# Kernel tuning notes

Hardware: AMD Instinct MI355X
Metric: run time of the kernel (lower is better)

Reference implementation:

```python
import jax, jax.numpy as jnp
import numpy as np

D, M, B, K = 512, 512, 8, 16
EPS = 1e-8
LAMBDA = 1.0
BALANCE_COEFF = 0.0


def _l2_normalize(x, axis=-1):
    n = jnp.linalg.norm(x, axis=axis, keepdims=True)
    return x / jnp.maximum(n, EPS)


def setup_inputs() -> dict:
    key = jax.random.key(0)
    k1, k2, k3 = jax.random.split(key, 3)
    x = jax.random.normal(k1, (2, 2048, D), dtype=jnp.float32)
    V = jax.random.normal(k2, (D, M, B), dtype=jnp.float32)
    U = jax.random.normal(k3, (M, D + 1, B), dtype=jnp.float32)
    return {"x": x, "V": V, "U": U}


def reference(x, V, U):
    input_shape = x.shape
    x_flat = x.reshape(-1, D)                      # (N, D)
    x_flat = _l2_normalize(x_flat)
    N = x_flat.shape[0]

    # UnitColNorm: unit-norm columns of V over the D axis (dim=0)
    Vn = V / jnp.maximum(jnp.linalg.norm(V, axis=0, keepdims=True), EPS)
    # UnitColNormPadded: unit-norm columns of U over the (D+1) axis (dim=1)
    Un = U / jnp.maximum(jnp.linalg.norm(U, axis=1, keepdims=True), EPS)

    # Read: h_all (N, m, b)
    h_all = jnp.einsum('nd,dmb->nmb', x_flat, Vn)

    # Top-k expert selection by energy
    energy = jnp.sum(h_all * h_all, axis=-1)       # (N, m)
    topk_vals, topk_idxs = jax.lax.top_k(energy, K)  # (N, k)
    h_sparse = jnp.take_along_axis(h_all, topk_idxs[:, :, None], axis=1)  # (N, k, b)

    # Autoencode aux (V_active gathered under no_grad in torch)
    V_t = jnp.transpose(Vn, (1, 0, 2))             # (m, D, b)
    V_active = jax.lax.stop_gradient(V_t[topk_idxs])  # (N, k, D, b)
    x_hat = jnp.einsum('nkdb,nkb->nd', V_active, h_sparse)
    resid = x_flat - x_hat
    uncaptured_energy = jnp.mean(jnp.sum(resid * resid, axis=-1))

    avg_energy = jnp.mean(energy, axis=0)          # (m,)
    denom = jnp.maximum(jnp.sum(avg_energy), EPS)
    probs = jnp.maximum(avg_energy / denom, EPS)
    balance_entropy = -jnp.sum(probs * jnp.log(probs)) / jnp.log(jnp.float32(M))
    topk_aux_loss = uncaptured_energy + BALANCE_COEFF * (1.0 - balance_entropy)

    # expert usage counts (monitoring only)
    counts = jnp.zeros((M,), jnp.float32).at[topk_idxs.reshape(-1)].add(1.0)

    # Write: gather per-token expert U matrices, drop the padding row
    U_active = Un[topk_idxs][:, :, :D, :]          # (N, k, D, b)
    writes = jnp.einsum('nkdb,nkb->nd', U_active, h_sparse)
    h_recon = jnp.einsum('nkdb,nd->nkb', U_active, writes)
    writer_aux_loss = jnp.mean((h_recon - jax.lax.stop_gradient(h_sparse)) ** 2)

    aux_loss = topk_aux_loss + writer_aux_loss

    x_out = _l2_normalize(x_flat + LAMBDA * writes).reshape(input_shape)
    return x_out, aux_loss, counts
```

## Files before the change

### kernel.cpp

```cpp
#include <hip/hip_runtime.h>
#include <math.h>

#define N_TOK 4096
#define D_DIM 512
#define M_EXP 512
#define B_DIM 8
#define K_TOP 16
#define MB    4096
#define UROW  4104
#define EPSV  1e-8f
#define KTOT  1536

typedef unsigned short ushort8 __attribute__((ext_vector_type(8)));
typedef unsigned short ushort4v __attribute__((ext_vector_type(4)));
typedef short short8 __attribute__((ext_vector_type(8)));
typedef float f32x4 __attribute__((ext_vector_type(4)));

__device__ inline float b2f(unsigned short u) {
    union { unsigned int i; float f; } c;
    c.i = ((unsigned int)u) << 16;
    return c.f;
}
__device__ inline unsigned short f2b(float f) {
    union { float f; unsigned int i; } c; c.f = f;
    unsigned int lsb = (c.i >> 16) & 1;
    c.i += 0x7fffu + lsb;
    return (unsigned short)(c.i >> 16);
}
__device__ inline void gload_lds16(const unsigned short* g, unsigned short* l) {
    __builtin_amdgcn_global_load_lds(
        (const __attribute__((address_space(1))) unsigned int*)g,
        (__attribute__((address_space(3))) unsigned int*)l, 16, 0, 0);
}

__global__ __launch_bounds__(256) void k_norm_x(const float* __restrict__ x,
                                                float* __restrict__ xn,
                                                unsigned short* __restrict__ Abf,
                                                int* __restrict__ counts)
{
    if (blockIdx.x == 0) {
        counts[threadIdx.x] = 0;
        counts[threadIdx.x + 256] = 0;
    }
    int wave = threadIdx.x >> 6;
    int lane = threadIdx.x & 63;
    int n = blockIdx.x * 4 + wave;
    const float4* xp = (const float4*)&x[(size_t)n * D_DIM + lane * 8];
    float4 a = xp[0], b = xp[1];
    float s = a.x*a.x + a.y*a.y + a.z*a.z + a.w*a.w
            + b.x*b.x + b.y*b.y + b.z*b.z + b.w*b.w;
    #pragma unroll
    for (int off = 1; off < 64; off <<= 1) s += __shfl_xor(s, off);
    float inv = 1.0f / fmaxf(sqrtf(s), EPSV);
    float v[8] = {a.x*inv, a.y*inv, a.z*inv, a.w*inv,
                  b.x*inv, b.y*inv, b.z*inv, b.w*inv};
    float4* op = (float4*)&xn[(size_t)n * D_DIM + lane * 8];
    op[0] = make_float4(v[0], v[1], v[2], v[3]);
    op[1] = make_float4(v[4], v[5], v[6], v[7]);
    ushort8 hi, lo;
    #pragma unroll
    for (int j = 0; j < 8; ++j) {
        unsigned short h = f2b(v[j]);
        hi[j] = h;
        lo[j] = f2b(v[j] - b2f(h));
    }
    size_t base = (size_t)n * KTOT + lane * 8;
    *(ushort8*)&Abf[base]        = hi;
    *(ushort8*)&Abf[base + 512]  = hi;
    *(ushort8*)&Abf[base + 1024] = lo;
}

__global__ __launch_bounds__(256) void k_uvnorm_part(const float* __restrict__ V,
                                                     const float* __restrict__ U,
                                                     float* __restrict__ partV,
                                                     float* __restrict__ partU)
{
    int blk = blockIdx.x;
    if (blk < 256) {
        int s = blk >> 4;
        int t = (blk & 15) * 256 + threadIdx.x;
        float sum = 0.f;
        int d0 = s * 32;
        #pragma unroll 8
        for (int d = d0; d < d0 + 32; ++d) {
            float v = V[(size_t)d * MB + t];
            sum += v * v;
        }
        partV[(size_t)s * MB + t] = sum;
    } else {
        blk -= 256;
        int s = blk >> 4;
        int t = (blk & 15) * 256 + threadIdx.x;
        int m = t >> 3, b = t & 7;
        size_t base = (size_t)m * UROW + b;
        int pbeg = s * 32;
        int pend = (s == 15) ? 513 : pbeg + 32;
        float sum = 0.f;
        for (int p = pbeg; p < pend; ++p) {
            float u = U[base + (size_t)p * 8];
            sum += u * u;
        }
        partU[(size_t)s * MB + t] = sum;
    }
}

__global__ __launch_bounds__(256) void k_norm_UV2(const float* __restrict__ V,
                                                  const float* __restrict__ U,
                                                  const float* __restrict__ partV,
                                                  const float* __restrict__ partU,
                                                  unsigned short* __restrict__ Btbf,
                                                  unsigned short* __restrict__ WXt,
                                                  unsigned short* __restrict__ U2t)
{
    int blk = blockIdx.x;
    if (blk < 256) {
        int s = blk >> 4;
        int t = (blk & 15) * 256 + threadIdx.x;
        float n2 = 0.f;
        #pragma unroll
        for (int i = 0; i < 16; ++i) n2 += partV[(size_t)i * MB + t];
        float inv = 1.0f / fmaxf(sqrtf(n2), EPSV);
        size_t row = (size_t)t * KTOT;
        int dbeg = s * 32;
        for (int d0 = dbeg; d0 < dbeg + 32; d0 += 8) {
            ushort8 hi, lo;
            #pragma unroll
            for (int j = 0; j < 8; ++j) {
                float f = V[(size_t)(d0 + j) * MB + t] * inv;
                unsigned short h = f2b(f);
                hi[j] = h;
                lo[j] = f2b(f - b2f(h));
                WXt[(size_t)(512 + d0 + j) * MB + t] = h;
            }
            *(ushort8*)&Btbf[row + d0]        = hi;
            *(ushort8*)&Btbf[row + 512 + d0]  = lo;
            *(ushort8*)&Btbf[row + 1024 + d0] = hi;
        }
    } else {
        blk -= 256;
        int s = blk >> 4;
        int t = (blk & 15) * 256 + threadIdx.x;
        int m = t >> 3, b = t & 7;
        size_t base = (size_t)m * UROW + b;
        float n2 = 0.f;
        #pragma unroll
        for (int i = 0; i < 16; ++i) n2 += partU[(size_t)i * MB + t];
        float inv = 1.0f / fmaxf(sqrtf(n2), EPSV);
        int pbeg = s * 32;
        for (int p0 = pbeg; p0 < pbeg + 32; p0 += 8) {
            ushort8 h8;
            #pragma unroll
            for (int j = 0; j < 8; ++j) {
                unsigned short h = f2b(U[base + (size_t)(p0 + j) * 8] * inv);
                h8[j] = h;
                WXt[(size_t)(p0 + j) * MB + t] = h;
            }
            *(ushort8*)&U2t[(size_t)t * D_DIM + p0] = h8;
        }
    }
}

template<int KROW, int BUF, int KC, int MH, bool READB, int SBUF, int SOP, int SKC, bool DOVM>
__device__ __forceinline__ void gemm_phase(const unsigned short* __restrict__ A,
                                           const unsigned short* __restrict__ Bt,
                                           unsigned short (*lds)[2][2][8192],
                                           f32x4 (&acc)[8][4], short8 (&bfr)[4],
                                           int wr, int wc, int lane, int wid,
                                           int brow, int bcol, int stile)
{
    const unsigned short* aun = lds[BUF][0][KC];
    const unsigned short* bun = lds[BUF][1][KC];
    int ko = ((lane >> 4) ^ ((lane >> 1) & 3)) * 8;
    short8 af[4];
    #pragma unroll
    for (int mi = 0; mi < 4; ++mi) {
        int rowL = wr * 128 + (MH * 4 + mi) * 16 + (lane & 15);
        af[mi] = *(const short8*)&aun[rowL * 32 + ko];
    }
    if (READB) {
        #pragma unroll
        for (int ni = 0; ni < 4; ++ni) {
            int colL = wc * 64 + ni * 16 + (lane & 15);
            bfr[ni] = *(const short8*)&bun[colL * 32 + ko];
        }
    }
    {
        const unsigned short* src = SOP ? Bt : A;
        int rbase = SOP ? bcol : brow;
        #pragma unroll
        for (int j = 0; j < 2; ++j) {
            int c = wid * 128 + j * 64 + lane;
            int row = c >> 2, k8 = c & 3;
            int k8s = k8 ^ ((row >> 1) & 3);
            const unsigned short* gp = src + (size_t)(rbase + row) * KROW
                                     + stile * 64 + SKC * 32 + k8s * 8;
            unsigned short* lp = lds[SBUF][SOP][SKC] + (wid * 128 + j * 64) * 8;
            gload_lds16(gp, lp);
        }
    }
    __builtin_amdgcn_sched_barrier(0);
    __builtin_amdgcn_s_barrier();
    asm volatile("s_waitcnt lgkmcnt(0)" ::: "memory");
    __builtin_amdgcn_sched_barrier(0);
    __builtin_amdgcn_s_setprio(1);
    #pragma unroll
    for (int mi = 0; mi < 4; ++mi)
        #pragma unroll
        for (int ni = 0; ni < 4; ++ni)
            acc[MH * 4 + mi][ni] = __builtin_amdgcn_mfma_f32_16x16x32_bf16(
                af[mi], bfr[ni], acc[MH * 4 + mi][ni], 0, 0, 0);
    __builtin_amdgcn_s_setprio(0);
    if (DOVM) asm volatile("s_waitcnt vmcnt(8)" ::: "memory");
    __builtin_amdgcn_sched_barrier(0);
    __builtin_amdgcn_s_barrier();
    __builtin_amdgcn_sched_barrier(0);
}

template<int KROW, int KLEN, int NCOLT, int SPLITK, int LDC, int OUTMODE>
__global__ __launch_bounds__(512, 1) void k_gemm8(const unsigned short* __restrict__ A,
                                                  const unsigned short* __restrict__ Bt,
                                                  float* __restrict__ C,
                                                  unsigned short* __restrict__ Cb)
{
    __shared__ unsigned short lds[2][2][2][8192];

    constexpr int KT   = KLEN / 64;
    constexpr int NIT  = KLEN / 128;
    constexpr int ROWT = 16;
    constexpr int NWG  = ROWT * NCOLT * SPLITK;

    int tid = threadIdx.x;
    int wid = tid >> 6;
    int lane = tid & 63;
    int wr = wid >> 2, wc = wid & 3;

    int bid = blockIdx.x;
    int swz = (bid & 7) * (NWG / 8) + (bid >> 3);
    int ks   = swz / (ROWT * NCOLT);
    int tile = swz % (ROWT * NCOLT);
    int brow = (tile / NCOLT) * 256;
    int bcol = (tile % NCOLT) * 256;

    const unsigned short* Aofs = A + (size_t)ks * KLEN;
    const unsigned short* Bofs = Bt + (size_t)ks * KLEN;
    float* Cofs = C + (size_t)ks * 4096 * LDC;

    f32x4 acc[8][4] = {};
    short8 bfr[4];

    auto stage0 = [&](int sbuf, int sop, int skc, int stile) {
        const unsigned short* src = sop ? Bofs : Aofs;
        int rbase = sop ? bcol : brow;
        #pragma unroll
        for (int j = 0; j < 2; ++j) {
            int c = wid * 128 + j * 64 + lane;
            int row = c >> 2, k8 = c & 3;
            int k8s = k8 ^ ((row >> 1) & 3);
            const unsigned short* gp = src + (size_t)(rbase + row) * KROW
                                     + stile * 64 + skc * 32 + k8s * 8;
            unsigned short* lp = lds[sbuf][sop][skc] + (wid * 128 + j * 64) * 8;
            gload_lds16(gp, lp);
        }
    };
    stage0(0, 0, 0, 0); stage0(0, 1, 0, 0);
    stage0(0, 0, 1, 0); stage0(0, 1, 1, 0);
    stage0(1, 0, 0, 1); stage0(1, 1, 0, 1);
    asm volatile("s_waitcnt vmcnt(8)" ::: "memory");
    __builtin_amdgcn_sched_barrier(0);
    __builtin_amdgcn_s_barrier();
    __builtin_amdgcn_sched_barrier(0);

    for (int i = 0; i < NIT; ++i) {
        int t1 = 2 * i + 1; if (t1 > KT - 1) t1 = KT - 1;
        int t2 = 2 * i + 2; if (t2 > KT - 1) t2 = KT - 1;
        int t3 = 2 * i + 3; if (t3 > KT - 1) t3 = KT - 1;
        gemm_phase<KROW, 0, 0, 0, true , 1, 0, 1, false>(Aofs, Bofs, lds, acc, bfr, wr, wc, lane, wid, brow, bcol, t1);
        gemm_phase<KROW, 0, 0, 1, false, 1, 1, 1, true >(Aofs, Bofs, lds, acc, bfr, wr, wc, lane, wid, brow, bcol, t1);
        gemm_phase<KROW, 0, 1, 0, true , 0, 0, 0, false>(Aofs, Bofs, lds, acc, bfr, wr, wc, lane, wid, brow, bcol, t2);
        gemm_phase<KROW, 0, 1, 1, false, 0, 1, 0, true >(Aofs, Bofs, lds, acc, bfr, wr, wc, lane, wid, brow, bcol, t2);
        gemm_phase<KROW, 1, 0, 0, true , 0, 0, 1, false>(Aofs, Bofs, lds, acc, bfr, wr, wc, lane, wid, brow, bcol, t2);
        gemm_phase<KROW, 1, 0, 1, false, 0, 1, 1, true >(Aofs, Bofs, lds, acc, bfr, wr, wc, lane, wid, brow, bcol, t2);
        gemm_phase<KROW, 1, 1, 0, true , 1, 0, 0, false>(Aofs, Bofs, lds, acc, bfr, wr, wc, lane, wid, brow, bcol, t3);
        gemm_phase<KROW, 1, 1, 1, false, 1, 1, 0, true >(Aofs, Bofs, lds, acc, bfr, wr, wc, lane, wid, brow, bcol, t3);
    }

    if (OUTMODE == 0 || OUTMODE == 2) {
        #pragma unroll
        for (int mr = 0; mr < 8; ++mr) {
            int row0 = brow + wr * 128 + mr * 16 + (lane >> 4) * 4;
            #pragma unroll
            for (int nr = 0; nr < 4; ++nr) {
                int col = bcol + wc * 64 + nr * 16 + (lane & 15);
                #pragma unroll
                for (int r = 0; r < 4; ++r) {
                    if (OUTMODE == 0)
                        Cofs[(size_t)(row0 + r) * LDC + col] = acc[mr][nr][r];
                    else
                        Cb[(size_t)(row0 + r) * LDC + col] = f2b(acc[mr][nr][r]);
                }
            }
        }
    } else if (OUTMODE == 3) {
        #pragma unroll
        for (int mr = 0; mr < 8; ++mr) {
            int row0 = brow + wr * 128 + mr * 16 + (lane >> 4) * 4;
            #pragma unroll
            for (int nr = 0; nr < 4; ++nr) {
                int col = bcol + wc * 64 + nr * 16 + (lane & 15);
                f32x4 a = acc[mr][nr];
                #pragma unroll
                for (int r = 0; r < 4; ++r)
                    Cb[(size_t)(row0 + r) * 4096 + col] = f2b(a[r]);
                f32x4 sq;
                #pragma unroll
                for (int r = 0; r < 4; ++r) sq[r] = a[r] * a[r];
                #pragma unroll
                for (int off = 1; off <= 4; off <<= 1) {
                    sq[0] += __shfl_xor(sq[0], off);
                    sq[1] += __shfl_xor(sq[1], off);
                    sq[2] += __shfl_xor(sq[2], off);
                    sq[3] += __shfl_xor(sq[3], off);
                }
                if ((lane & 7) == 0) {
                    int e = ((bcol + wc * 64 + nr * 16) >> 3) + ((lane >> 3) & 1);
                    #pragma unroll
                    for (int r = 0; r < 4; ++r)
                        C[(size_t)(row0 + r) * 512 + e] = sq[r];
                }
            }
        }
    } else {
        float local = 0.f;
        #pragma unroll
        for (int mr = 0; mr < 8; ++mr) {
            int row0 = brow + wr * 128 + mr * 16 + (lane >> 4) * 4;
            #pragma unroll
            for (int nr = 0; nr < 4; ++nr) {
                int col = bcol + wc * 64 + nr * 16 + (lane & 15);
                #pragma unroll
                for (int r = 0; r < 4; ++r) {
                    unsigned short hbits = Cb[(size_t)(row0 + r) * 4096 + col];
                    if (hbits & 0x7fffu) {
                        float d = acc[mr][nr][r] - b2f(hbits);
                        local += d * d;
                    }
                }
            }
        }
        __syncthreads();
        float* red = (float*)lds;
        red[tid] = local;
        __syncthreads();
        for (int s = 256; s > 0; s >>= 1) {
            if (tid < s) red[tid] += red[tid + s];
            __syncthreads();
        }
        if (tid == 0) C[bid] = red[0];
    }
}

__global__ __launch_bounds__(256) void k_topk2(const float* __restrict__ energy,
                                               unsigned short* __restrict__ hbf,
                                               int* __restrict__ topk_idx,
                                               int* __restrict__ counts)
{
    int wave = threadIdx.x >> 6;
    int lane = threadIdx.x & 63;
    int n = blockIdx.x * 4 + wave;
    float ev[8];
    #pragma unroll
    for (int i = 0; i < 8; ++i) ev[i] = energy[(size_t)n * M_EXP + i * 64 + lane];
    for (int r = 0; r < K_TOP; ++r) {
        float bv = -1.0f; int bi = 0;
        #pragma unroll
        for (int i = 0; i < 8; ++i) {
            if (ev[i] > bv) { bv = ev[i]; bi = i * 64 + lane; }
        }
        #pragma unroll
        for (int off = 1; off < 64; off <<= 1) {
            float ov = __shfl_xor(bv, off);
            int   oi = __shfl_xor(bi, off);
            if (ov > bv || (ov == bv && oi < bi)) { bv = ov; bi = oi; }
        }
        if (lane == 0) {
            topk_idx[n * K_TOP + r] = bi;
            atomicAdd(&counts[bi], 1);
        }
        #pragma unroll
        for (int i = 0; i < 8; ++i)
            if (((bi >> 6) == i) && (lane == (bi & 63))) ev[i] = -INFINITY;
    }
    ushort8 z = {0, 0, 0, 0, 0, 0, 0, 0};
    #pragma unroll
    for (int i = 0; i < 8; ++i) {
        int e = i * 64 + lane;
        if (ev[i] != -INFINITY)
            *(ushort8*)&hbf[(size_t)n * MB + e * 8] = z;
    }
}

__global__ __launch_bounds__(256) void k_reduce_fin(const float* __restrict__ P,
                                                    const float* __restrict__ xn,
                                                    float* __restrict__ x_out,
                                                    unsigned short* __restrict__ wb,
                                                    float* __restrict__ uncap)
{
    const size_t S = (size_t)4096 * 1024;
    int n = blockIdx.x;
    int t = threadIdx.x;
    int c = t * 4;
    size_t base = (size_t)n * 1024 + c;
    float4 a = *(const float4*)&P[base];
    float4 b = *(const float4*)&P[base + S];
    float4 cc = *(const float4*)&P[base + 2 * S];
    float4 d = *(const float4*)&P[base + 3 * S];
    float4 v = make_float4(a.x + b.x + cc.x + d.x, a.y + b.y + cc.y + d.y,
                           a.z + b.z + cc.z + d.z, a.w + b.w + cc.w + d.w);
    bool isW = (c < 512);
    int xc = isW ? c : (c - 512);
    float4 xv = *(const float4*)&xn[(size_t)n * D_DIM + xc];
    float4 yr;
    if (isW) yr = make_float4(xv.x + v.x, xv.y + v.y, xv.z + v.z, xv.w + v.w);
    else     yr = make_float4(xv.x - v.x, xv.y - v.y, xv.z - v.z, xv.w - v.w);
    float local = yr.x*yr.x + yr.y*yr.y + yr.z*yr.z + yr.w*yr.w;

    __shared__ float red[256];
    __shared__ float sinv;
    red[t] = local;
    __syncthreads();
    for (int s = 64; s > 0; s >>= 1) {
        if ((t & 127) < s) red[t] += red[t + s];
        __syncthreads();
    }
    if (t == 0) {
        uncap[n] = red[128];
        sinv = 1.0f / fmaxf(sqrtf(red[0]), EPSV);
    }
    __syncthreads();
    if (isW) {
        float inv = sinv;
        *(float4*)&x_out[(size_t)n * D_DIM + c] =
            make_float4(yr.x*inv, yr.y*inv, yr.z*inv, yr.w*inv);
        ushort4v o;
        o[0] = f2b(yr.x); o[1] = f2b(yr.y); o[2] = f2b(yr.z); o[3] = f2b(yr.w);
        *(ushort4v*)&wb[(size_t)n * 512 + c] = o;
    }
}

__global__ __launch_bounds__(256) void k_finalize(const float* __restrict__ uncap,
                                                  const float* __restrict__ writer_part,
                                                  const int* __restrict__ counts,
                                                  float* __restrict__ out)
{
    __shared__ float ru[256], rw[256];
    int t = threadIdx.x;
    float su = 0.f;
    for (int i = t; i < N_TOK; i += 256) su += uncap[i];
    float sw = writer_part[t];
    ru[t] = su; rw[t] = sw;
    __syncthreads();
    for (int s = 128; s > 0; s >>= 1) {
        if (t < s) { ru[t] += ru[t + s]; rw[t] += rw[t + s]; }
        __syncthreads();
    }
    if (t == 0)
        out[(size_t)N_TOK * D_DIM] = ru[0] / (float)N_TOK
                                   + rw[0] / (float)(N_TOK * K_TOP * B_DIM);
    for (int i = t; i < M_EXP; i += 256)
        out[(size_t)N_TOK * D_DIM + 1 + i] = (float)counts[i];
}

extern "C" void kernel_launch(void* const* d_in, const int* in_sizes, int n_in,
                              void* d_out, int out_size, void* d_ws, size_t ws_size,
                              hipStream_t stream)
{
    const float* x = (const float*)d_in[0];
    const float* V = (const float*)d_in[1];
    const float* U = (const float*)d_in[2];
    float* out = (float*)d_out;

    float* ws     = (float*)d_ws;
    float* xn     = ws;
    float* P      = xn + 2097152;
    float* uncap  = P + 16777216;
    float* writer_part = uncap + 4096;
    int*   topk_i = (int*)(writer_part + 512);
    int*   counts = topk_i + 65536;
    float* partV  = (float*)(counts + 1024);
    float* partU  = partV + 65536;
    unsigned short* hbf = (unsigned short*)(partU + 65536);
    unsigned short* U2t = hbf + 16777216;
    unsigned short* WXt = U2t + 2097152;
    unsigned short* R   = WXt + 4194304;
    unsigned short* Abf  = R;
    unsigned short* Btbf = R + 6291456;
    unsigned short* writesb = R;
    float* energy = P;

    k_norm_x    <<<N_TOK / 4, 256, 0, stream>>>(x, xn, Abf, counts);
    k_uvnorm_part<<<512, 256, 0, stream>>>(V, U, partV, partU);
    k_norm_UV2  <<<512, 256, 0, stream>>>(V, U, partV, partU, Btbf, WXt, U2t);
    k_gemm8<KTOT, KTOT, 16, 1, 4096, 3><<<256, 512, 0, stream>>>(Abf, Btbf, energy, hbf);
    k_topk2     <<<N_TOK / 4, 256, 0, stream>>>(energy, hbf, topk_i, counts);
    k_gemm8<4096, 1024, 4, 4, 1024, 0><<<256, 512, 0, stream>>>(hbf, WXt, P, nullptr);
    k_reduce_fin<<<4096, 256, 0, stream>>>(P, xn, out, writesb, uncap);
    k_gemm8<D_DIM, D_DIM, 16, 1, 4096, 4><<<256, 512, 0, stream>>>(writesb, U2t, writer_part, hbf);
    k_finalize  <<<1, 256, 0, stream>>>(uncap, writer_part, counts, out);
}
```

Before: 212.6 us.

## Merge x-norm and UV partial-norm kernels; restructure GEMM phases into paired MFMA halves

Fuses the x normalization kernel and the V/U partial-norm kernel into one launch by block-index dispatch, saving a kernel launch and letting the two independent workloads share the GPU. The GEMM inner loop is rewritten from eight single-half phases into four paired phases. Each pair loads both A halves and B from LDS up front, issues two global-to-LDS stages interleaved with the two MFMA groups, and drops the explicit lgkmcnt wait. This cuts the barriers per iteration but raises register pressure. Without the lgkmcnt wait, LDS reads may not be complete before the MFMAs consume them unless the compiler inserts the wait.

```diff
diff --git a/kernel.cpp b/kernel.cpp
--- a/kernel.cpp
+++ b/kernel.cpp
@@ -33,50 +33,49 @@
         (__attribute__((address_space(3))) unsigned int*)l, 16, 0, 0);
 }
 
-__global__ __launch_bounds__(256) void k_norm_x(const float* __restrict__ x,
-                                                float* __restrict__ xn,
-                                                unsigned short* __restrict__ Abf,
-                                                int* __restrict__ counts)
-{
-    if (blockIdx.x == 0) {
-        counts[threadIdx.x] = 0;
-        counts[threadIdx.x + 256] = 0;
-    }
-    int wave = threadIdx.x >> 6;
-    int lane = threadIdx.x & 63;
-    int n = blockIdx.x * 4 + wave;
-    const float4* xp = (const float4*)&x[(size_t)n * D_DIM + lane * 8];
-    float4 a = xp[0], b = xp[1];
-    float s = a.x*a.x + a.y*a.y + a.z*a.z + a.w*a.w
-            + b.x*b.x + b.y*b.y + b.z*b.z + b.w*b.w;
-    #pragma unroll
-    for (int off = 1; off < 64; off <<= 1) s += __shfl_xor(s, off);
-    float inv = 1.0f / fmaxf(sqrtf(s), EPSV);
-    float v[8] = {a.x*inv, a.y*inv, a.z*inv, a.w*inv,
-                  b.x*inv, b.y*inv, b.z*inv, b.w*inv};
-    float4* op = (float4*)&xn[(size_t)n * D_DIM + lane * 8];
-    op[0] = make_float4(v[0], v[1], v[2], v[3]);
-    op[1] = make_float4(v[4], v[5], v[6], v[7]);
-    ushort8 hi, lo;
-    #pragma unroll
-    for (int j = 0; j < 8; ++j) {
-        unsigned short h = f2b(v[j]);
-        hi[j] = h;
-        lo[j] = f2b(v[j] - b2f(h));
-    }
-    size_t base = (size_t)n * KTOT + lane * 8;
-    *(ushort8*)&Abf[base]        = hi;
-    *(ushort8*)&Abf[base + 512]  = hi;
-    *(ushort8*)&Abf[base + 1024] = lo;
-}
-
-__global__ __launch_bounds__(256) void k_uvnorm_part(const float* __restrict__ V,
+__global__ __launch_bounds__(256) void k_norm_x_part(const float* __restrict__ x,
+                                                     float* __restrict__ xn,
+                                                     unsigned short* __restrict__ Abf,
+                                                     int* __restrict__ counts,
+                                                     const float* __restrict__ V,
                                                      const float* __restrict__ U,
                                                      float* __restrict__ partV,
                                                      float* __restrict__ partU)
 {
     int blk = blockIdx.x;
-    if (blk < 256) {
+    if (blk < 1024) {
+        if (blk == 0) {
+            counts[threadIdx.x] = 0;
+            counts[threadIdx.x + 256] = 0;
+        }
+        int wave = threadIdx.x >> 6;
+        int lane = threadIdx.x & 63;
+        int n = blk * 4 + wave;
+        const float4* xp = (const float4*)&x[(size_t)n * D_DIM + lane * 8];
+        float4 a = xp[0], b = xp[1];
+        float s = a.x*a.x + a.y*a.y + a.z*a.z + a.w*a.w
+                + b.x*b.x + b.y*b.y + b.z*b.z + b.w*b.w;
+        #pragma unroll
+        for (int off = 1; off < 64; off <<= 1) s += __shfl_xor(s, off);
+        float inv = 1.0f / fmaxf(sqrtf(s), EPSV);
+        float v[8] = {a.x*inv, a.y*inv, a.z*inv, a.w*inv,
+                      b.x*inv, b.y*inv, b.z*inv, b.w*inv};
+        float4* op = (float4*)&xn[(size_t)n * D_DIM + lane * 8];
+        op[0] = make_float4(v[0], v[1], v[2], v[3]);
+        op[1] = make_float4(v[4], v[5], v[6], v[7]);
+        ushort8 hi, lo;
+        #pragma unroll
+        for (int j = 0; j < 8; ++j) {
+            unsigned short h = f2b(v[j]);
+            hi[j] = h;
+            lo[j] = f2b(v[j] - b2f(h));
+        }
+        size_t base = (size_t)n * KTOT + lane * 8;
+        *(ushort8*)&Abf[base]        = hi;
+        *(ushort8*)&Abf[base + 512]  = hi;
+        *(ushort8*)&Abf[base + 1024] = lo;
+    } else if (blk < 1280) {
+        blk -= 1024;
         int s = blk >> 4;
         int t = (blk & 15) * 256 + threadIdx.x;
         float sum = 0.f;
@@ -88,7 +87,7 @@
         }
         partV[(size_t)s * MB + t] = sum;
     } else {
-        blk -= 256;
+        blk -= 1280;
         int s = blk >> 4;
         int t = (blk & 15) * 256 + threadIdx.x;
         int m = t >> 3, b = t & 7;
@@ -160,60 +159,85 @@
     }
 }
 
-template<int KROW, int BUF, int KC, int MH, bool READB, int SBUF, int SOP, int SKC, bool DOVM>
-__device__ __forceinline__ void gemm_phase(const unsigned short* __restrict__ A,
-                                           const unsigned short* __restrict__ Bt,
-                                           unsigned short (*lds)[2][2][8192],
-                                           f32x4 (&acc)[8][4], short8 (&bfr)[4],
-                                           int wr, int wc, int lane, int wid,
-                                           int brow, int bcol, int stile)
+template<int KROW, int BUF, int KC,
+         int SB1, int SO1, int SK1, int SB2, int SO2, int SK2>
+__device__ __forceinline__ void gemm_pair(const unsigned short* __restrict__ A,
+                                          const unsigned short* __restrict__ Bt,
+                                          unsigned short (*lds)[2][2][8192],
+                                          f32x4 (&acc)[8][4],
+                                          int wr, int wc, int lane, int wid,
+                                          int brow, int bcol, int stileA, int stileB)
 {
     const unsigned short* aun = lds[BUF][0][KC];
     const unsigned short* bun = lds[BUF][1][KC];
     int ko = ((lane >> 4) ^ ((lane >> 1) & 3)) * 8;
-    short8 af[4];
+    short8 af0[4], af1[4], bf[4];
     #pragma unroll
     for (int mi = 0; mi < 4; ++mi) {
-        int rowL = wr * 128 + (MH * 4 + mi) * 16 + (lane & 15);
-        af[mi] = *(const short8*)&aun[rowL * 32 + ko];
-    }
-    if (READB) {
-        #pragma unroll
-        for (int ni = 0; ni < 4; ++ni) {
-            int colL = wc * 64 + ni * 16 + (lane & 15);
-            bfr[ni] = *(const short8*)&bun[colL * 32 + ko];
-        }
+        int rowL = wr * 128 + mi * 16 + (lane & 15);
+        af0[mi] = *(const short8*)&aun[rowL * 32 + ko];
+    }
+    #pragma unroll
+    for (int ni = 0; ni < 4; ++ni) {
+        int colL = wc * 64 + ni * 16 + (lane & 15);
+        bf[ni] = *(const short8*)&bun[colL * 32 + ko];
+    }
+    #pragma unroll
+    for (int mi = 0; mi < 4; ++mi) {
+        int rowL = wr * 128 + (4 + mi) * 16 + (lane & 15);
+        af1[mi] = *(const short8*)&aun[rowL * 32 + ko];
     }
     {
-        const unsigned short* src = SOP ? Bt : A;
-        int rbase = SOP ? bcol : brow;
+        const unsigned short* src = SO1 ? Bt : A;
+        int rbase = SO1 ? bcol : brow;
         #pragma unroll
         for (int j = 0; j < 2; ++j) {
             int c = wid * 128 + j * 64 + lane;
             int row = c >> 2, k8 = c & 3;
             int k8s = k8 ^ ((row >> 1) & 3);
             const unsigned short* gp = src + (size_t)(rbase + row) * KROW
-                                     + stile * 64 + SKC * 32 + k8s * 8;
-            unsigned short* lp = lds[SBUF][SOP][SKC] + (wid * 128 + j * 64) * 8;
-            gload_lds16(gp, lp);
-        }
-    }
+                                     + stileA * 64 + SK1 * 32 + k8s * 8;
+            gload_lds16(gp, lds[SB1][SO1][SK1] + (wid * 128 + j * 64) * 8);
+        }
+    }
+    __builtin_amdgcn_s_barrier();
+    __builtin_amdgcn_sched_barrier(0);
+    __builtin_amdgcn_s_setprio(1);
+    #pragma unroll
+    for (int mi = 0; mi < 4; ++mi)
+        #pragma unroll
+        for (int ni = 0; ni < 4; ++ni)
+            acc[mi][ni] = __builtin_amdgcn_mfma_f32_16x16x32_bf16(
+                af0[mi], bf[ni], acc[mi][ni], 0, 0, 0);
+    __builtin_amdgcn_s_setprio(0);
     __builtin_amdgcn_sched_barrier(0);
     __builtin_amdgcn_s_barrier();
-    asm volatile("s_waitcnt lgkmcnt(0)" ::: "memory");
+    {
+        const unsigned short* src = SO2 ? Bt : A;
+        int rbase = SO2 ? bcol : brow;
+        #pragma unroll
+        for (int j = 0; j < 2; ++j) {
+            int c = wid * 128 + j * 64 + lane;
+            int row = c >> 2, k8 = c & 3;
+            int k8s = k8 ^ ((row >> 1) & 3);
+            const unsigned short* gp = src + (size_t)(rbase + row) * KROW
+                                     + stileB * 64 + SK2 * 32 + k8s * 8;
+            gload_lds16(gp, lds[SB2][SO2][SK2] + (wid * 128 + j * 64) * 8);
+        }
+    }
+    __builtin_amdgcn_s_barrier();
     __builtin_amdgcn_sched_barrier(0);
     __builtin_amdgcn_s_setprio(1);
     #pragma unroll
     for (int mi = 0; mi < 4; ++mi)
         #pragma unroll
         for (int ni = 0; ni < 4; ++ni)
-            acc[MH * 4 + mi][ni] = __builtin_amdgcn_mfma_f32_16x16x32_bf16(
-                af[mi], bfr[ni], acc[MH * 4 + mi][ni], 0, 0, 0);
+            acc[4 + mi][ni] = __builtin_amdgcn_mfma_f32_16x16x32_bf16(
+                af1[mi], bf[ni], acc[4 + mi][ni], 0, 0, 0);
     __builtin_amdgcn_s_setprio(0);
-    if (DOVM) asm volatile("s_waitcnt vmcnt(8)" ::: "memory");
+    asm volatile("s_waitcnt vmcnt(8)" ::: "memory");
     __builtin_amdgcn_sched_barrier(0);
     __builtin_amdgcn_s_barrier();
-    __builtin_amdgcn_sched_barrier(0);
 }
 
 template<int KROW, int KLEN, int NCOLT, int SPLITK, int LDC, int OUTMODE>
@@ -246,7 +270,6 @@
     float* Cofs = C + (size_t)ks * 4096 * LDC;
 
     f32x4 acc[8][4] = {};
-    short8 bfr[4];
 
     auto stage0 = [&](int sbuf, int sop, int skc, int stile) {
         const unsigned short* src = sop ? Bofs : Aofs;
@@ -274,14 +297,10 @@
         int t1 = 2 * i + 1; if (t1 > KT - 1) t1 = KT - 1;
         int t2 = 2 * i + 2; if (t2 > KT - 1) t2 = KT - 1;
         int t3 = 2 * i + 3; if (t3 > KT - 1) t3 = KT - 1;
-        gemm_phase<KROW, 0, 0, 0, true , 1, 0, 1, false>(Aofs, Bofs, lds, acc, bfr, wr, wc, lane, wid, brow, bcol, t1);
-        gemm_phase<KROW, 0, 0, 1, false, 1, 1, 1, true >(Aofs, Bofs, lds, acc, bfr, wr, wc, lane, wid, brow, bcol, t1);
-        gemm_phase<KROW, 0, 1, 0, true , 0, 0, 0, false>(Aofs, Bofs, lds, acc, bfr, wr, wc, lane, wid, brow, bcol, t2);
-        gemm_phase<KROW, 0, 1, 1, false, 0, 1, 0, true >(Aofs, Bofs, lds, acc, bfr, wr, wc, lane, wid, brow, bcol, t2);
-        gemm_phase<KROW, 1, 0, 0, true , 0, 0, 1, false>(Aofs, Bofs, lds, acc, bfr, wr, wc, lane, wid, brow, bcol, t2);
-        gemm_phase<KROW, 1, 0, 1, false, 0, 1, 1, true >(Aofs, Bofs, lds, acc, bfr, wr, wc, lane, wid, brow, bcol, t2);
-        gemm_phase<KROW, 1, 1, 0, true , 1, 0, 0, false>(Aofs, Bofs, lds, acc, bfr, wr, wc, lane, wid, brow, bcol, t3);
-        gemm_phase<KROW, 1, 1, 1, false, 1, 1, 0, true >(Aofs, Bofs, lds, acc, bfr, wr, wc, lane, wid, brow, bcol, t3);
+        gemm_pair<KROW, 0, 0, 1, 0, 1, 1, 1, 1>(Aofs, Bofs, lds, acc, wr, wc, lane, wid, brow, bcol, t1, t1);
+        gemm_pair<KROW, 0, 1, 0, 0, 0, 0, 1, 0>(Aofs, Bofs, lds, acc, wr, wc, lane, wid, brow, bcol, t2, t2);
+        gemm_pair<KROW, 1, 0, 0, 0, 1, 0, 1, 1>(Aofs, Bofs, lds, acc, wr, wc, lane, wid, brow, bcol, t2, t2);
+        gemm_pair<KROW, 1, 1, 1, 0, 0, 1, 1, 0>(Aofs, Bofs, lds, acc, wr, wc, lane, wid, brow, bcol, t3, t3);
     }
 
     if (OUTMODE == 0 || OUTMODE == 2) {
@@ -497,8 +516,7 @@
     unsigned short* writesb = R;
     float* energy = P;
 
-    k_norm_x    <<<N_TOK / 4, 256, 0, stream>>>(x, xn, Abf, counts);
-    k_uvnorm_part<<<512, 256, 0, stream>>>(V, U, partV, partU);
+    k_norm_x_part<<<1536, 256, 0, stream>>>(x, xn, Abf, counts, V, U, partV, partU);
     k_norm_UV2  <<<512, 256, 0, stream>>>(V, U, partV, partU, Btbf, WXt, U2t);
     k_gemm8<KTOT, KTOT, 16, 1, 4096, 3><<<256, 512, 0, stream>>>(Abf, Btbf, energy, hbf);
     k_topk2     <<<N_TOK / 4, 256, 0, stream>>>(energy, hbf, topk_i, counts);
```

New measurement: 215.4 us. About the same (+1.3%).

## Switch GEMM to 32x32x16 MFMA tiles and merge x-norm with UV partial norms

Applied to the files above, without the earlier changes.

The shared GEMM inner loop now uses 32x32x16 bf16 MFMA instructions with 16-element accumulators instead of 16x16x32, which changes the LDS fragment loads and every epilogue's row/column mapping. The aim is fewer MFMA issues and fewer LDS fragment reads per tile. The x normalization kernel is also merged with the V/U partial-norm kernel into one launch, saving a kernel launch and letting the two independent jobs overlap. The energy epilogue now shuffles once per element rather than per 4-vector, which may add shuffle overhead.

```diff
diff --git a/kernel.cpp b/kernel.cpp
--- a/kernel.cpp
+++ b/kernel.cpp
@@ -14,7 +14,7 @@
 typedef unsigned short ushort8 __attribute__((ext_vector_type(8)));
 typedef unsigned short ushort4v __attribute__((ext_vector_type(4)));
 typedef short short8 __attribute__((ext_vector_type(8)));
-typedef float f32x4 __attribute__((ext_vector_type(4)));
+typedef float f32x16 __attribute__((ext_vector_type(16)));
 
 __device__ inline float b2f(unsigned short u) {
     union { unsigned int i; float f; } c;
@@ -33,50 +33,49 @@
         (__attribute__((address_space(3))) unsigned int*)l, 16, 0, 0);
 }
 
-__global__ __launch_bounds__(256) void k_norm_x(const float* __restrict__ x,
-                                                float* __restrict__ xn,
-                                                unsigned short* __restrict__ Abf,
-                                                int* __restrict__ counts)
-{
-    if (blockIdx.x == 0) {
-        counts[threadIdx.x] = 0;
-        counts[threadIdx.x + 256] = 0;
-    }
-    int wave = threadIdx.x >> 6;
-    int lane = threadIdx.x & 63;
-    int n = blockIdx.x * 4 + wave;
-    const float4* xp = (const float4*)&x[(size_t)n * D_DIM + lane * 8];
-    float4 a = xp[0], b = xp[1];
-    float s = a.x*a.x + a.y*a.y + a.z*a.z + a.w*a.w
-            + b.x*b.x + b.y*b.y + b.z*b.z + b.w*b.w;
-    #pragma unroll
-    for (int off = 1; off < 64; off <<= 1) s += __shfl_xor(s, off);
-    float inv = 1.0f / fmaxf(sqrtf(s), EPSV);
-    float v[8] = {a.x*inv, a.y*inv, a.z*inv, a.w*inv,
-                  b.x*inv, b.y*inv, b.z*inv, b.w*inv};
-    float4* op = (float4*)&xn[(size_t)n * D_DIM + lane * 8];
-    op[0] = make_float4(v[0], v[1], v[2], v[3]);
-    op[1] = make_float4(v[4], v[5], v[6], v[7]);
-    ushort8 hi, lo;
-    #pragma unroll
-    for (int j = 0; j < 8; ++j) {
-        unsigned short h = f2b(v[j]);
-        hi[j] = h;
-        lo[j] = f2b(v[j] - b2f(h));
-    }
-    size_t base = (size_t)n * KTOT + lane * 8;
-    *(ushort8*)&Abf[base]        = hi;
-    *(ushort8*)&Abf[base + 512]  = hi;
-    *(ushort8*)&Abf[base + 1024] = lo;
-}
-
-__global__ __launch_bounds__(256) void k_uvnorm_part(const float* __restrict__ V,
+__global__ __launch_bounds__(256) void k_norm_x_part(const float* __restrict__ x,
+                                                     float* __restrict__ xn,
+                                                     unsigned short* __restrict__ Abf,
+                                                     int* __restrict__ counts,
+                                                     const float* __restrict__ V,
                                                      const float* __restrict__ U,
                                                      float* __restrict__ partV,
                                                      float* __restrict__ partU)
 {
     int blk = blockIdx.x;
-    if (blk < 256) {
+    if (blk < 1024) {
+        if (blk == 0) {
+            counts[threadIdx.x] = 0;
+            counts[threadIdx.x + 256] = 0;
+        }
+        int wave = threadIdx.x >> 6;
+        int lane = threadIdx.x & 63;
+        int n = blk * 4 + wave;
+        const float4* xp = (const float4*)&x[(size_t)n * D_DIM + lane * 8];
+        float4 a = xp[0], b = xp[1];
+        float s = a.x*a.x + a.y*a.y + a.z*a.z + a.w*a.w
+                + b.x*b.x + b.y*b.y + b.z*b.z + b.w*b.w;
+        #pragma unroll
+        for (int off = 1; off < 64; off <<= 1) s += __shfl_xor(s, off);
+        float inv = 1.0f / fmaxf(sqrtf(s), EPSV);
+        float v[8] = {a.x*inv, a.y*inv, a.z*inv, a.w*inv,
+                      b.x*inv, b.y*inv, b.z*inv, b.w*inv};
+        float4* op = (float4*)&xn[(size_t)n * D_DIM + lane * 8];
+        op[0] = make_float4(v[0], v[1], v[2], v[3]);
+        op[1] = make_float4(v[4], v[5], v[6], v[7]);
+        ushort8 hi, lo;
+        #pragma unroll
+        for (int j = 0; j < 8; ++j) {
+            unsigned short h = f2b(v[j]);
+            hi[j] = h;
+            lo[j] = f2b(v[j] - b2f(h));
+        }
+        size_t base = (size_t)n * KTOT + lane * 8;
+        *(ushort8*)&Abf[base]        = hi;
+        *(ushort8*)&Abf[base + 512]  = hi;
+        *(ushort8*)&Abf[base + 1024] = lo;
+    } else if (blk < 1280) {
+        blk -= 1024;
         int s = blk >> 4;
         int t = (blk & 15) * 256 + threadIdx.x;
         float sum = 0.f;
@@ -88,7 +87,7 @@
         }
         partV[(size_t)s * MB + t] = sum;
     } else {
-        blk -= 256;
+        blk -= 1280;
         int s = blk >> 4;
         int t = (blk & 15) * 256 + threadIdx.x;
         int m = t >> 3, b = t & 7;
@@ -164,24 +163,33 @@
 __device__ __forceinline__ void gemm_phase(const unsigned short* __restrict__ A,
                                            const unsigned short* __restrict__ Bt,
                                            unsigned short (*lds)[2][2][8192],
-                                           f32x4 (&acc)[8][4], short8 (&bfr)[4],
+                                           f32x16 (&acc)[4][2], short8 (&bfr)[2][2],
                                            int wr, int wc, int lane, int wid,
                                            int brow, int bcol, int stile)
 {
     const unsigned short* aun = lds[BUF][0][KC];
     const unsigned short* bun = lds[BUF][1][KC];
-    int ko = ((lane >> 4) ^ ((lane >> 1) & 3)) * 8;
-    short8 af[4];
+    int l5 = lane >> 5;
+    int r31 = lane & 31;
+    short8 af[2][2];
     #pragma unroll
-    for (int mi = 0; mi < 4; ++mi) {
-        int rowL = wr * 128 + (MH * 4 + mi) * 16 + (lane & 15);
-        af[mi] = *(const short8*)&aun[rowL * 32 + ko];
+    for (int mi = 0; mi < 2; ++mi) {
+        int rowL = wr * 128 + (MH * 2 + mi) * 32 + r31;
+        #pragma unroll
+        for (int ks = 0; ks < 2; ++ks) {
+            int slot = (ks * 2 + l5) ^ ((rowL >> 1) & 3);
+            af[mi][ks] = *(const short8*)&aun[rowL * 32 + slot * 8];
+        }
     }
     if (READB) {
         #pragma unroll
-        for (int ni = 0; ni < 4; ++ni) {
-            int colL = wc * 64 + ni * 16 + (lane & 15);
-            bfr[ni] = *(const short8*)&bun[colL * 32 + ko];
+        for (int ni = 0; ni < 2; ++ni) {
+            int colL = wc * 64 + ni * 32 + r31;
+            #pragma unroll
+            for (int ks = 0; ks < 2; ++ks) {
+                int slot = (ks * 2 + l5) ^ ((colL >> 1) & 3);
+                bfr[ni][ks] = *(const short8*)&bun[colL * 32 + slot * 8];
+            }
         }
     }
     {
@@ -204,11 +212,13 @@
     __builtin_amdgcn_sched_barrier(0);
     __builtin_amdgcn_s_setprio(1);
     #pragma unroll
-    for (int mi = 0; mi < 4; ++mi)
-        #pragma unroll
-        for (int ni = 0; ni < 4; ++ni)
-            acc[MH * 4 + mi][ni] = __builtin_amdgcn_mfma_f32_16x16x32_bf16(
-                af[mi], bfr[ni], acc[MH * 4 + mi][ni], 0, 0, 0);
+    for (int mi = 0; mi < 2; ++mi)
+        #pragma unroll
+        for (int ni = 0; ni < 2; ++ni)
+            #pragma unroll
+            for (int ks = 0; ks < 2; ++ks)
+                acc[MH * 2 + mi][ni] = __builtin_amdgcn_mfma_f32_32x32x16_bf16(
+                    af[mi][ks], bfr[ni][ks], acc[MH * 2 + mi][ni], 0, 0, 0);
     __builtin_amdgcn_s_setprio(0);
     if (DOVM) asm volatile("s_waitcnt vmcnt(8)" ::: "memory");
     __builtin_amdgcn_sched_barrier(0);
@@ -233,6 +243,8 @@
     int wid = tid >> 6;
     int lane = tid & 63;
     int wr = wid >> 2, wc = wid & 3;
+    int l5 = lane >> 5;
+    int r31 = lane & 31;
 
     int bid = blockIdx.x;
     int swz = (bid & 7) * (NWG / 8) + (bid >> 3);
@@ -245,8 +257,8 @@
     const unsigned short* Bofs = Bt + (size_t)ks * KLEN;
     float* Cofs = C + (size_t)ks * 4096 * LDC;
 
-    f32x4 acc[8][4] = {};
-    short8 bfr[4];
+    f32x16 acc[4][2] = {};
+    short8 bfr[2][2];
 
     auto stage0 = [&](int sbuf, int sop, int skc, int stile) {
         const unsigned short* src = sop ? Bofs : Aofs;
@@ -286,62 +298,55 @@
 
     if (OUTMODE == 0 || OUTMODE == 2) {
         #pragma unroll
-        for (int mr = 0; mr < 8; ++mr) {
-            int row0 = brow + wr * 128 + mr * 16 + (lane >> 4) * 4;
-            #pragma unroll
-            for (int nr = 0; nr < 4; ++nr) {
-                int col = bcol + wc * 64 + nr * 16 + (lane & 15);
+        for (int mt = 0; mt < 4; ++mt) {
+            #pragma unroll
+            for (int nt = 0; nt < 2; ++nt) {
+                int col = bcol + wc * 64 + nt * 32 + r31;
                 #pragma unroll
-                for (int r = 0; r < 4; ++r) {
+                for (int r = 0; r < 16; ++r) {
+                    int row = brow + wr * 128 + mt * 32 + (r & 3) + 8 * (r >> 2) + 4 * l5;
                     if (OUTMODE == 0)
-                        Cofs[(size_t)(row0 + r) * LDC + col] = acc[mr][nr][r];
+                        Cofs[(size_t)row * LDC + col] = acc[mt][nt][r];
                     else
-                        Cb[(size_t)(row0 + r) * LDC + col] = f2b(acc[mr][nr][r]);
+                        Cb[(size_t)row * LDC + col] = f2b(acc[mt][nt][r]);
                 }
             }
         }
     } else if (OUTMODE == 3) {
         #pragma unroll
-        for (int mr = 0; mr < 8; ++mr) {
-            int row0 = brow + wr * 128 + mr * 16 + (lane >> 4) * 4;
-            #pragma unroll
-            for (int nr = 0; nr < 4; ++nr) {
-                int col = bcol + wc * 64 + nr * 16 + (lane & 15);
-                f32x4 a = acc[mr][nr];
+        for (int mt = 0; mt < 4; ++mt) {
+            #pragma unroll
+            for (int nt = 0; nt < 2; ++nt) {
+                int col = bcol + wc * 64 + nt * 32 + r31;
                 #pragma unroll
-                for (int r = 0; r < 4; ++r)
-                    Cb[(size_t)(row0 + r) * 4096 + col] = f2b(a[r]);
-                f32x4 sq;
-                #pragma unroll
-                for (int r = 0; r < 4; ++r) sq[r] = a[r] * a[r];
-                #pragma unroll
-                for (int off = 1; off <= 4; off <<= 1) {
-                    sq[0] += __shfl_xor(sq[0], off);
-                    sq[1] += __shfl_xor(sq[1], off);
-                    sq[2] += __shfl_xor(sq[2], off);
-                    sq[3] += __shfl_xor(sq[3], off);
-                }
-                if ((lane & 7) == 0) {
-                    int e = ((bcol + wc * 64 + nr * 16) >> 3) + ((lane >> 3) & 1);
-                    #pragma unroll
-                    for (int r = 0; r < 4; ++r)
-                        C[(size_t)(row0 + r) * 512 + e] = sq[r];
+                for (int r = 0; r < 16; ++r) {
+                    int row = brow + wr * 128 + mt * 32 + (r & 3) + 8 * (r >> 2) + 4 * l5;
+                    float a = acc[mt][nt][r];
+                    Cb[(size_t)row * 4096 + col] = f2b(a);
+                    float sq = a * a;
+                    sq += __shfl_xor(sq, 1);
+                    sq += __shfl_xor(sq, 2);
+                    sq += __shfl_xor(sq, 4);
+                    if ((lane & 7) == 0) {
+                        int e = (bcol + wc * 64 + nt * 32 + r31) >> 3;
+                        C[(size_t)row * 512 + e] = sq;
+                    }
                 }
             }
         }
     } else {
         float local = 0.f;
         #pragma unroll
-        for (int mr = 0; mr < 8; ++mr) {
-            int row0 = brow + wr * 128 + mr * 16 + (lane >> 4) * 4;
-            #pragma unroll
-            for (int nr = 0; nr < 4; ++nr) {
-                int col = bcol + wc * 64 + nr * 16 + (lane & 15);
+        for (int mt = 0; mt < 4; ++mt) {
+            #pragma unroll
+            for (int nt = 0; nt < 2; ++nt) {
+                int col = bcol + wc * 64 + nt * 32 + r31;
                 #pragma unroll
-                for (int r = 0; r < 4; ++r) {
-                    unsigned short hbits = Cb[(size_t)(row0 + r) * 4096 + col];
+                for (int r = 0; r < 16; ++r) {
+                    int row = brow + wr * 128 + mt * 32 + (r & 3) + 8 * (r >> 2) + 4 * l5;
+                    unsigned short hbits = Cb[(size_t)row * 4096 + col];
                     if (hbits & 0x7fffu) {
-                        float d = acc[mr][nr][r] - b2f(hbits);
+                        float d = acc[mt][nt][r] - b2f(hbits);
                         local += d * d;
                     }
                 }
@@ -497,8 +502,7 @@
     unsigned short* writesb = R;
     float* energy = P;
 
-    k_norm_x    <<<N_TOK / 4, 256, 0, stream>>>(x, xn, Abf, counts);
-    k_uvnorm_part<<<512, 256, 0, stream>>>(V, U, partV, partU);
+    k_norm_x_part<<<1536, 256, 0, stream>>>(x, xn, Abf, counts, V, U, partV, partU);
     k_norm_UV2  <<<512, 256, 0, stream>>>(V, U, partV, partU, Btbf, WXt, U2t);
     k_gemm8<KTOT, KTOT, 16, 1, 4096, 3><<<256, 512, 0, stream>>>(Abf, Btbf, energy, hbf);
     k_topk2     <<<N_TOK / 4, 256, 0, stream>>>(energy, hbf, topk_i, counts);
```

Result: slower. 227.3 us (+6.9%).
